# Kernel tuning notes

Hardware: AMD Instinct MI355X
Metric: run time of the kernel (lower is better)

Reference implementation:

```python
import jax, jax.numpy as jnp
import numpy as np

B, S, D, H = 2, 2048, 1024, 16
HD = D // H                      # 64
NUM_ROPE_DIMS = 2
NF = HD // (2 * NUM_ROPE_DIMS)   # 16 freqs per rope dim -> total HD//2
FFN_H = 4 * D


def householder_matrix(vs):
    """Product of Householder reflections: Q = prod_i (I - 2 v_i v_i^T / ||v_i||^2)."""
    dim = vs.shape[-1]
    def step(Q, v):
        v = v[:, None]
        Q = Q - (2.0 / (jnp.sum(v * v) + 1e-8)) * (v @ (v.T @ Q))
        return Q, None
    Q, _ = jax.lax.scan(step, jnp.eye(dim, dtype=vs.dtype), vs)
    return Q


def rmsnorm(x):
    # torch.nn.RMSNorm(eps=None) uses dtype eps, no affine
    return x * jax.lax.rsqrt(jnp.mean(x * x, axis=-1, keepdims=True) + jnp.finfo(x.dtype).eps)


def setup_inputs() -> dict:
    key = jax.random.key(0)
    ks = jax.random.split(key, 8)
    x = jax.random.normal(ks[0], (B, S, D), jnp.float32)
    mask = jnp.tril(jnp.ones((S, S), dtype=bool))          # causal block mask
    qkv_w = jax.random.normal(ks[1], (3 * D, D), jnp.float32) * 0.02
    out_w = jax.random.normal(ks[2], (D, D), jnp.float32) * 0.02
    gate_w = jax.random.normal(ks[3], (D, D), jnp.float32) * 0.02
    gate_b = jnp.zeros((D,), jnp.float32)
    w12 = jax.random.normal(ks[4], (2 * FFN_H, D), jnp.float32) * 0.02
    w3 = jax.random.normal(ks[5], (D, FFN_H), jnp.float32) * 0.02
    hh_vs = jax.random.normal(ks[6], (HD // 2, HD), jnp.float32) * 0.02
    inv_freq = 1.0 / (10000.0 ** (jnp.arange(NF, dtype=jnp.float32) / NF))
    pos = jnp.arange(S, dtype=jnp.float32)
    rope_pos = jnp.stack([pos, pos], axis=-1)              # [S, num_rope_dims]
    return dict(x=x, mask=mask, qkv_w=qkv_w, out_w=out_w, gate_w=gate_w,
                gate_b=gate_b, w12=w12, w3=w3, hh_vs=hh_vs,
                inv_freq=inv_freq, rope_pos=rope_pos)


def reference(x, mask, qkv_w, out_w, gate_w, gate_b, w12, w3, hh_vs, inv_freq, rope_pos):
    Bs, Ss, Ds = x.shape
    resid = x
    xn = rmsnorm(x)
    qkv = xn @ qkv_w.T                                      # [B,S,3D]
    q, k, v = jnp.split(qkv, 3, axis=-1)
    q = q.reshape(Bs, Ss, H, HD).transpose(0, 2, 1, 3)      # [B,H,S,HD]
    k = k.reshape(Bs, Ss, H, HD).transpose(0, 2, 1, 3)
    v = v.reshape(Bs, Ss, H, HD).transpose(0, 2, 1, 3)

    # RnRoPE: rotate into canonical basis, apply RoPE, rotate back
    Q = householder_matrix(hh_vs)                           # [HD,HD]
    q = q @ Q.T
    k = k @ Q.T
    # geo_state.scale = 1.0
    full = jnp.einsum('sd,f->sdf', rope_pos, inv_freq).reshape(Ss, -1)  # [S, HD//2]
    half = HD // 2
    full = full[:, :half]
    emb = jnp.concatenate([full, full], axis=-1)            # [S, HD]
    cos, sin = jnp.cos(emb), jnp.sin(emb)

    def rot(t):
        t1, t2 = jnp.split(t, 2, axis=-1)
        return t * cos + jnp.concatenate([-t2, t1], axis=-1) * sin

    q = rot(q) @ Q
    k = rot(k) @ Q

    # block-masked attention (flex_attention default scale = 1/sqrt(HD))
    scores = jnp.einsum('bhsd,bhtd->bhst', q, k) / jnp.sqrt(jnp.asarray(HD, x.dtype))
    scores = jnp.where(mask, scores, -jnp.inf)
    attn = jax.nn.softmax(scores, axis=-1)
    o = jnp.einsum('bhst,bhtd->bhsd', attn, v)
    o = o.transpose(0, 2, 1, 3).reshape(Bs, Ss, Ds)
    o = o @ out_w.T
    gate = jax.nn.sigmoid(o @ gate_w.T + gate_b)
    x = resid + o * gate

    # SwiGLU FFN
    resid2 = x
    xn2 = rmsnorm(x)
    x12 = xn2 @ w12.T
    x1, x2 = jnp.split(x12, 2, axis=-1)
    ffn = (jax.nn.silu(x1) * x2) @ w3.T
    return resid2 + ffn
```

## Files before the change

### kernel.cpp

```cpp
#include <hip/hip_runtime.h>
#include <hip/hip_bf16.h>
#include <math.h>

constexpr int Bc = 2, Sc = 2048, Dc = 1024, Hc = 16, HDc = 64;
constexpr int D3 = 3 * Dc;

typedef __bf16 bf16x8 __attribute__((ext_vector_type(8)));
typedef float f32x4 __attribute__((ext_vector_type(4)));

__device__ __forceinline__ void gll16(const void* g, void* l) {
  __builtin_amdgcn_global_load_lds((const __attribute__((address_space(1))) unsigned int*)g,
                                   (__attribute__((address_space(3))) unsigned int*)l,
                                   16, 0, 0);
}

__device__ __forceinline__ unsigned short f2bf(float v) {
  __hip_bfloat16 h = __float2bfloat16(v);
  return *(unsigned short*)&h;
}
__device__ __forceinline__ float b2f(unsigned short u) {
  unsigned v = ((unsigned)u) << 16;
  return __uint_as_float(v);
}

#define SBAR() asm volatile("s_barrier" ::: "memory")

__global__ __launch_bounds__(64) void hh_kernel(const float* __restrict__ vs,
                                                float* __restrict__ Qout) {
  __shared__ float Qm[64][65];
  __shared__ float vsh[64];
  int t = threadIdx.x;
  for (int i = 0; i < 64; ++i) Qm[i][t] = (i == t) ? 1.0f : 0.0f;
  for (int it = 0; it < 32; ++it) {
    __syncthreads();
    vsh[t] = vs[it * 64 + t];
    __syncthreads();
    float nv = 0.0f;
    for (int i = 0; i < 64; ++i) nv += vsh[i] * vsh[i];
    float c = 2.0f / (nv + 1e-8f);
    float wj = 0.0f;
    for (int i = 0; i < 64; ++i) wj += vsh[i] * Qm[i][t];
    for (int i = 0; i < 64; ++i) Qm[i][t] -= c * vsh[i] * wj;
  }
  __syncthreads();
  for (int i = 0; i < 64; ++i) Qout[i * 64 + t] = Qm[i][t];
}

__global__ __launch_bounds__(256) void prep_kernel(const float* __restrict__ qkv_w,
                                                   const float* __restrict__ out_w,
                                                   const float* __restrict__ w3,
                                                   const float* __restrict__ gate_w,
                                                   const float* __restrict__ rope_pos,
                                                   const float* __restrict__ inv_freq,
                                                   const float* __restrict__ Qm,
                                                   float2* __restrict__ rtab,
                                                   unsigned short* __restrict__ wqkvb,
                                                   unsigned short* __restrict__ woutb,
                                                   unsigned short* __restrict__ w3b,
                                                   unsigned short* __restrict__ wgateb) {
  const int blk = blockIdx.x;
  const int t = threadIdx.x;
  if (blk < 256) {
    int id = blk * 256 + t;
    int s = id >> 5, d = id & 31;
    float pos = rope_pos[s * 2 + (d >> 4)];
    float emb = pos * inv_freq[d & 15];
    rtab[id] = make_float2(cosf(emb), sinf(emb));
  } else if (blk < 512) {
    __shared__ float qs[64 * 64];
    const int gid = blk - 256;
    const int g = gid >> 3;
    const int c = gid & 7;
    const int base = g * 64;
#pragma unroll
    for (int i = 0; i < 16; ++i) qs[t + i * 256] = Qm[t + i * 256];
    __syncthreads();
    const int tj = t & 127;
    const int rh = (t >> 7) * 32;
    const int col = c * 128 + tj;
    float acc[32] = {};
    const float* wp = qkv_w + (size_t)base * 1024 + col;
    for (int e = 0; e < 64; ++e) {
      float wv = wp[(size_t)e * 1024];
#pragma unroll
      for (int r = 0; r < 32; ++r) acc[r] += qs[(rh + r) * 64 + e] * wv;
    }
    const float sc = (base < 1024) ? 0.18033688f : 1.0f;
#pragma unroll
    for (int r = 0; r < 32; ++r)
      wqkvb[(size_t)(base + rh + r) * 1024 + col] = f2bf(acc[r] * sc);
  } else {
    const float* in;
    unsigned short* out;
    int i;
    if (blk < 1536) {
      in = qkv_w + (size_t)2048 * 1024;
      out = wqkvb + (size_t)2048 * 1024;
      i = (blk - 512) * 256 + t;
    } else if (blk < 2560) {
      in = out_w; out = woutb;
      i = (blk - 1536) * 256 + t;
    } else if (blk < 6656) {
      in = w3; out = w3b;
      i = (blk - 2560) * 256 + t;
    } else {
      in = gate_w; out = wgateb;
      i = (blk - 6656) * 256 + t;
    }
    float4 v = ((const float4*)in)[i];
    ushort4 o;
    o.x = f2bf(v.x); o.y = f2bf(v.y); o.z = f2bf(v.z); o.w = f2bf(v.w);
    ((ushort4*)out)[i] = o;
  }
}

__device__ __forceinline__ void rms_body(const float* __restrict__ in,
                                         unsigned short* __restrict__ out, int row, int t) {
  const float4* x4 = (const float4*)(in + (size_t)row * Dc);
  float4 v = x4[t];
  float s = v.x * v.x + v.y * v.y + v.z * v.z + v.w * v.w;
#pragma unroll
  for (int off = 1; off < 64; off <<= 1) s += __shfl_xor(s, off);
  __shared__ float wsum[4];
  if ((t & 63) == 0) wsum[t >> 6] = s;
  __syncthreads();
  float tot = wsum[0] + wsum[1] + wsum[2] + wsum[3];
  float r = rsqrtf(tot * (1.0f / Dc) + 1.1920928955078125e-07f);
  ushort4 o;
  o.x = f2bf(v.x * r); o.y = f2bf(v.y * r); o.z = f2bf(v.z * r); o.w = f2bf(v.w * r);
  ((ushort4*)(out + (size_t)row * Dc))[t] = o;
}

__global__ __launch_bounds__(256) void rmsnorm_bf16_kernel(const float* __restrict__ in,
                                                           unsigned short* __restrict__ out) {
  rms_body(in, out, blockIdx.x, threadIdx.x);
}

__global__ __launch_bounds__(256) void ropevt_kernel(const unsigned short* __restrict__ qkv,
                                                     const float2* __restrict__ tab,
                                                     unsigned short* __restrict__ qb,
                                                     unsigned short* __restrict__ kb,
                                                     unsigned short* __restrict__ vtb) {
  __shared__ unsigned short tile[64 * 72];
  const int blk = blockIdx.x;
  const int t = threadIdx.x;
  if (blk < 2048) {
    int gid = blk * 64 + (t >> 2);
    int sub = t & 3;
    int h = gid & 15;
    int which = (gid >> 4) & 1;
    int tok = gid >> 5;
    int s = tok & (Sc - 1), b = tok >> 11;
    const unsigned short* src = qkv + (size_t)tok * D3 + which * Dc + h * 64 + sub * 8;
    uint4 lov = *(const uint4*)src;
    uint4 hiv = *(const uint4*)(src + 32);
    const unsigned short* lp = (const unsigned short*)&lov;
    const unsigned short* hp = (const unsigned short*)&hiv;
    unsigned short olo[8], ohi[8];
    const float2* tp = tab + s * 32 + sub * 8;
#pragma unroll
    for (int i = 0; i < 8; ++i) {
      float2 cs = tp[i];
      float lo = b2f(lp[i]), hi = b2f(hp[i]);
      olo[i] = f2bf(lo * cs.x - hi * cs.y);
      ohi[i] = f2bf(hi * cs.x + lo * cs.y);
    }
    unsigned short* dst = (which ? kb : qb) + ((size_t)((b * Hc + h) * Sc + s)) * 64 + sub * 8;
    *(uint4*)dst = *(uint4*)olo;
    *(uint4*)(dst + 32) = *(uint4*)ohi;
  } else {
    int v = blk - 2048;
    int st = v & 31;
    int bh = v >> 5;
    int b = bh >> 4, h = bh & 15;
    int srow = t >> 2, c16 = (t & 3) * 16;
    const unsigned short* src =
        qkv + (size_t)(b * Sc + st * 64 + srow) * D3 + 2 * Dc + h * 64 + c16;
    uint4 a0 = *(const uint4*)src;
    uint4 a1 = *(const uint4*)(src + 8);
    *(uint4*)(tile + srow * 72 + c16) = a0;
    *(uint4*)(tile + srow * 72 + c16 + 8) = a1;
    __syncthreads();
    int d = t >> 2, sch = (t & 3) * 16;
    unsigned short tmp[16];
#pragma unroll
    for (int i = 0; i < 16; ++i) tmp[i] = tile[(sch + i) * 72 + d];
    unsigned short* dst = vtb + ((size_t)(bh * 64 + d)) * Sc + st * 64 + sch;
    *(uint4*)dst = *(uint4*)tmp;
    *(uint4*)(dst + 8) = *(uint4*)(tmp + 8);
  }
}

template <int MODE>
__global__ __launch_bounds__(512, 1) void mgemm8p(const unsigned short* __restrict__ A,
                                                  const unsigned short* __restrict__ B,
                                                  unsigned short* __restrict__ C,
                                                  int M, int N, int K) {
  __shared__ unsigned short lds[65536];
  const int t = threadIdx.x;
  const int lane = t & 63;
  const int wave = t >> 6;
  const int wr = wave >> 2, wc = wave & 3;
  const int l15 = lane & 15, l4 = lane >> 4;
  const int gx = gridDim.x;
  const int nwg = gx * gridDim.y;
  const int id = blockIdx.y * gx + blockIdx.x;
  const int swz = (id & 7) * (nwg >> 3) + (id >> 3);
  const int m0 = (swz / gx) * 256;
  const int n0 = (swz % gx) * 256;
  const int NT = K >> 6;
  const int sko = (((t & 3) ^ ((t >> 3) & 3)) * 8);
  const unsigned short* ag0 = A + (size_t)(m0 + (t >> 2)) * K + sko;
  const unsigned short* ag1 = ag0 + (size_t)128 * K;
  const unsigned short* bg0 = B + (size_t)(n0 + (t >> 2)) * K + sko;
  const unsigned short* bg1 = bg0 + (size_t)128 * K;
  const int t8 = t * 8;
  const int ks = (l4 ^ ((l15 >> 1) & 3)) * 8;
  gll16(ag0, lds + t8);
  gll16(ag1, lds + 4096 + t8);
  gll16(bg0, lds + 32768 + t8);
  gll16(bg1, lds + 32768 + 4096 + t8);
  gll16(ag0 + 32, lds + 8192 + t8);
  gll16(ag1 + 32, lds + 8192 + 4096 + t8);
  gll16(bg0 + 32, lds + 32768 + 8192 + t8);
  gll16(bg1 + 32, lds + 32768 + 8192 + 4096 + t8);
  asm volatile("s_waitcnt vmcnt(4)" ::: "memory");
  SBAR();
  f32x4 acc[8][4] = {};
  for (int kt = 0; kt < NT; ++kt) {
    const int cur = (kt & 1) << 14;
    const int nxt = cur ^ 16384;
    const int kof = ((kt + 1 < NT) ? (kt + 1) : kt) << 6;
    const unsigned short* Ap = lds + cur;
    const unsigned short* Bp = lds + 32768 + cur;
    bf16x8 a[8], b0, b1;
#pragma unroll
    for (int i = 0; i < 8; ++i)
      a[i] = *(const bf16x8*)(Ap + (wr * 128 + i * 16 + l15) * 32 + ks);
    b0 = *(const bf16x8*)(Bp + (wc * 64 + l15) * 32 + ks);
    b1 = *(const bf16x8*)(Bp + (wc * 64 + 16 + l15) * 32 + ks);
    gll16(ag0 + kof, lds + nxt + t8);
    gll16(ag1 + kof, lds + nxt + 4096 + t8);
    SBAR();
    __builtin_amdgcn_s_setprio(1);
#pragma unroll
    for (int i = 0; i < 8; ++i) {
      acc[i][0] = __builtin_amdgcn_mfma_f32_16x16x32_bf16(a[i], b0, acc[i][0], 0, 0, 0);
      acc[i][1] = __builtin_amdgcn_mfma_f32_16x16x32_bf16(a[i], b1, acc[i][1], 0, 0, 0);
    }
    __builtin_amdgcn_s_setprio(0);
    SBAR();
    b0 = *(const bf16x8*)(Bp + (wc * 64 + 32 + l15) * 32 + ks);
    b1 = *(const bf16x8*)(Bp + (wc * 64 + 48 + l15) * 32 + ks);
    gll16(bg0 + kof, lds + 32768 + nxt + t8);
    gll16(bg1 + kof, lds + 32768 + nxt + 4096 + t8);
    asm volatile("s_waitcnt vmcnt(4)" ::: "memory");
    SBAR();
    __builtin_amdgcn_s_setprio(1);
#pragma unroll
    for (int i = 0; i < 8; ++i) {
      acc[i][2] = __builtin_amdgcn_mfma_f32_16x16x32_bf16(a[i], b0, acc[i][2], 0, 0, 0);
      acc[i][3] = __builtin_amdgcn_mfma_f32_16x16x32_bf16(a[i], b1, acc[i][3], 0, 0, 0);
    }
    __builtin_amdgcn_s_setprio(0);
    SBAR();
#pragma unroll
    for (int i = 0; i < 8; ++i)
      a[i] = *(const bf16x8*)(Ap + 8192 + (wr * 128 + i * 16 + l15) * 32 + ks);
    b0 = *(const bf16x8*)(Bp + 8192 + (wc * 64 + l15) * 32 + ks);
    b1 = *(const bf16x8*)(Bp + 8192 + (wc * 64 + 16 + l15) * 32 + ks);
    gll16(ag0 + kof + 32, lds + nxt + 8192 + t8);
    gll16(ag1 + kof + 32, lds + nxt + 8192 + 4096 + t8);
    SBAR();
    __builtin_amdgcn_s_setprio(1);
#pragma unroll
    for (int i = 0; i < 8; ++i) {
      acc[i][0] = __builtin_amdgcn_mfma_f32_16x16x32_bf16(a[i], b0, acc[i][0], 0, 0, 0);
      acc[i][1] = __builtin_amdgcn_mfma_f32_16x16x32_bf16(a[i], b1, acc[i][1], 0, 0, 0);
    }
    __builtin_amdgcn_s_setprio(0);
    SBAR();
    b0 = *(const bf16x8*)(Bp + 8192 + (wc * 64 + 32 + l15) * 32 + ks);
    b1 = *(const bf16x8*)(Bp + 8192 + (wc * 64 + 48 + l15) * 32 + ks);
    gll16(bg0 + kof + 32, lds + 32768 + nxt + 8192 + t8);
    gll16(bg1 + kof + 32, lds + 32768 + nxt + 8192 + 4096 + t8);
    asm volatile("s_waitcnt vmcnt(4)" ::: "memory");
    SBAR();
    __builtin_amdgcn_s_setprio(1);
#pragma unroll
    for (int i = 0; i < 8; ++i) {
      acc[i][2] = __builtin_amdgcn_mfma_f32_16x16x32_bf16(a[i], b0, acc[i][2], 0, 0, 0);
      acc[i][3] = __builtin_amdgcn_mfma_f32_16x16x32_bf16(a[i], b1, acc[i][3], 0, 0, 0);
    }
    __builtin_amdgcn_s_setprio(0);
    SBAR();
  }
  asm volatile("s_waitcnt vmcnt(0)" ::: "memory");
  const int r0 = m0 + wr * 128 + l4 * 4;
  if (MODE == 0) {
    const int c0 = n0 + wc * 64 + l15;
#pragma unroll
    for (int i = 0; i < 8; ++i)
#pragma unroll
      for (int j = 0; j < 4; ++j)
#pragma unroll
        for (int r = 0; r < 4; ++r)
          C[(size_t)(r0 + i * 16 + r) * N + c0 + j * 16] = f2bf(acc[i][j][r]);
  } else {
    const int nc = N >> 1;
    const int c0 = (n0 >> 1) + wc * 32 + l15;
#pragma unroll
    for (int i = 0; i < 8; ++i)
#pragma unroll
      for (int p = 0; p < 2; ++p)
#pragma unroll
        for (int r = 0; r < 4; ++r) {
          float v = acc[i][2 * p][r];
          float sv = v / (1.0f + __expf(-v));
          C[(size_t)(r0 + i * 16 + r) * nc + c0 + p * 16] = f2bf(sv * acc[i][2 * p + 1][r]);
        }
  }
}

template <int MODE>
__global__ __launch_bounds__(256, 2) void mgemm64(const unsigned short* __restrict__ A,
                                                  const unsigned short* __restrict__ W,
                                                  const float* __restrict__ R,
                                                  const float* __restrict__ R2,
                                                  const float* __restrict__ bias,
                                                  void* __restrict__ Cout,
                                                  void* __restrict__ Cout2,
                                                  int M, int N, int K) {
  __shared__ unsigned short As[3][2][2048];
  __shared__ unsigned short Bs[3][2][4096];
  const int t = threadIdx.x;
  const int lane = t & 63;
  const int wave = t >> 6;
  const int wr = wave >> 1, wc = wave & 1;
  const int gx = gridDim.x;
  const int nwg = gx * gridDim.y;
  const int id = blockIdx.y * gx + blockIdx.x;
  const int swz = (id & 7) * (nwg >> 3) + (id >> 3);
  const int m0 = (swz / gx) * 64, n0 = (swz % gx) * 128;
  f32x4 acc[2][4] = {};
  const int srow = t >> 2;
  const int sch = (((t & 3) ^ ((t >> 3) & 3)) * 8);
  const unsigned short* Ag = A + (size_t)(m0 + srow) * K + sch;
  const unsigned short* Wg = W + (size_t)(n0 + srow) * K + sch;
  const size_t rstep = (size_t)64 * K;
  const int frow = lane & 15;
  const int l4 = lane >> 4;
  const int fk = (l4 ^ ((frow >> 1) & 3)) * 8;
  const int t8 = t * 8;
#pragma unroll
  for (int p = 0; p < 2; ++p) {
    const int ko = p * 64;
    gll16(Ag + ko, As[p][0] + t8);
    gll16(Ag + ko + 32, As[p][1] + t8);
    gll16(Wg + ko, Bs[p][0] + t8);
    gll16(Wg + ko + rstep, Bs[p][0] + 2048 + t8);
    gll16(Wg + ko + 32, Bs[p][1] + t8);
    gll16(Wg + ko + rstep + 32, Bs[p][1] + 2048 + t8);
  }
  const int NS = K >> 6;
  for (int s = 0; s < NS; ++s) {
    const int cur = s % 3;
    const int nxt = (s + 2) % 3;
    const int kn = (s + 2 < NS) ? (s + 2) * 64 : s * 64;
    gll16(Ag + kn, As[nxt][0] + t8);
    gll16(Ag + kn + 32, As[nxt][1] + t8);
    gll16(Wg + kn, Bs[nxt][0] + t8);
    gll16(Wg + kn + rstep, Bs[nxt][0] + 2048 + t8);
    gll16(Wg + kn + 32, Bs[nxt][1] + t8);
    gll16(Wg + kn + rstep + 32, Bs[nxt][1] + 2048 + t8);
    asm volatile("s_waitcnt vmcnt(12)" ::: "memory");
    SBAR();
#pragma unroll
    for (int kh = 0; kh < 2; ++kh) {
      bf16x8 af[2], bq[4];
#pragma unroll
      for (int i = 0; i < 2; ++i)
        af[i] = *(const bf16x8*)(As[cur][kh] + (wr * 32 + i * 16 + frow) * 32 + fk);
#pragma unroll
      for (int j = 0; j < 4; ++j)
        bq[j] = *(const bf16x8*)(Bs[cur][kh] + (wc * 64 + j * 16 + frow) * 32 + fk);
      __builtin_amdgcn_s_setprio(1);
#pragma unroll
      for (int i = 0; i < 2; ++i)
#pragma unroll
        for (int j = 0; j < 4; ++j)
          acc[i][j] = __builtin_amdgcn_mfma_f32_16x16x32_bf16(af[i], bq[j], acc[i][j], 0, 0, 0);
      __builtin_amdgcn_s_setprio(0);
    }
    SBAR();
  }
  asm volatile("s_waitcnt vmcnt(0)" ::: "memory");
  const int crow = wr * 32 + (lane >> 4) * 4;
  const int ccol = wc * 64 + (lane & 15);
#pragma unroll
  for (int i = 0; i < 2; ++i) {
#pragma unroll
    for (int j = 0; j < 4; ++j) {
#pragma unroll
      for (int r = 0; r < 4; ++r) {
        int row = m0 + crow + i * 16 + r;
        int col = n0 + ccol + j * 16;
        float v = acc[i][j][r];
        size_t off = (size_t)row * N + col;
        if (MODE == 2) {
          ((float*)Cout)[off] = v + R[off];
        } else if (MODE == 4) {
          ((float*)Cout)[off] = v;
          ((unsigned short*)Cout2)[off] = f2bf(v);
        } else {
          float g = v + bias[col];
          float sg = 1.0f / (1.0f + __expf(-g));
          ((float*)Cout)[off] = R[off] + R2[off] * sg;
        }
      }
    }
  }
}

__global__ __launch_bounds__(256, 3) void mattn(const unsigned short* __restrict__ qb,
                                                const unsigned short* __restrict__ kb,
                                                const unsigned short* __restrict__ vtb,
                                                unsigned short* __restrict__ opart,
                                                float* __restrict__ lpart,
                                                const float* __restrict__ w12,
                                                unsigned short* __restrict__ w12b) {
  __shared__ unsigned short Ks[2][4096];
  __shared__ unsigned short Vts[2][4096];
  __shared__ unsigned short Ps[4 * 16 * 72];
  const int t = threadIdx.x;
  if (blockIdx.x >= 40) {
    const int r = (blockIdx.x - 40) * 32 + blockIdx.y;
    const int g = r >> 5, u = r & 31;
    const int src = ((u < 16) ? 0 : 4096) + g * 16 + (u & 15);
    float4 v = ((const float4*)(w12 + (size_t)src * 1024))[t];
    ushort4 o;
    o.x = f2bf(v.x); o.y = f2bf(v.y); o.z = f2bf(v.z); o.w = f2bf(v.w);
    ((ushort4*)(w12b + (size_t)r * 1024))[t] = o;
    return;
  }
  const int bidx = 39 - blockIdx.x;
  int qt, s;
  if (bidx < 4)       { qt = bidx;                  s = 0; }
  else if (bidx < 12) { qt = 4 + ((bidx - 4) >> 1); s = (bidx - 4) & 1; }
  else if (bidx < 24) { int u = bidx - 12; int q3 = u / 3; qt = 8 + q3; s = u - 3 * q3; }
  else                { qt = 12 + ((bidx - 24) >> 2); s = (bidx - 24) & 3; }
  const int nt = 2 * qt + 2;
  const int kt0 = s * 8;
  const int kt1 = (kt0 + 8 < nt) ? kt0 + 8 : nt;
  const int bh = blockIdx.y;
  const int lane = t & 63, w = t >> 6;
  const int l15 = lane & 15, l4 = lane >> 4;
  const unsigned short* qbase = qb + ((size_t)bh * Sc + qt * 128) * 64;
  const unsigned short* kbase = kb + (size_t)bh * Sc * 64;
  const unsigned short* vbase = vtb + (size_t)bh * 64 * Sc;
  bf16x8 qf[2][2];
#pragma unroll
  for (int ch = 0; ch < 2; ++ch)
#pragma unroll
    for (int kc = 0; kc < 2; ++kc)
      qf[ch][kc] = *(const bf16x8*)(qbase + (size_t)(ch * 64 + w * 16 + l15) * 64 +
                                    (kc * 4 + l4) * 8);
  const int sr = t >> 3;
  const int scg = (t & 7) ^ (sr & 7);
  gll16(kbase + (size_t)(kt0 * 64 + sr) * 64 + scg * 8, Ks[0] + t * 8);
  gll16(kbase + (size_t)(kt0 * 64 + sr + 32) * 64 + scg * 8, Ks[0] + 2048 + t * 8);
  gll16(vbase + (size_t)sr * Sc + kt0 * 64 + scg * 8, Vts[0] + t * 8);
  gll16(vbase + (size_t)(sr + 32) * Sc + kt0 * 64 + scg * 8, Vts[0] + 2048 + t * 8);
  f32x4 oacc[2][4] = {};
  float lrow[2][4] = {};
  unsigned short* pw = Ps + w * 16 * 72;
  for (int kt = kt0; kt < kt1; ++kt) {
    const int cur = (kt - kt0) & 1;
    const int ktn = (kt + 1 < kt1) ? kt + 1 : kt;
    gll16(kbase + (size_t)(ktn * 64 + sr) * 64 + scg * 8, Ks[cur ^ 1] + t * 8);
    gll16(kbase + (size_t)(ktn * 64 + sr + 32) * 64 + scg * 8, Ks[cur ^ 1] + 2048 + t * 8);
    gll16(vbase + (size_t)sr * Sc + ktn * 64 + scg * 8, Vts[cur ^ 1] + t * 8);
    gll16(vbase + (size_t)(sr + 32) * Sc + ktn * 64 + scg * 8, Vts[cur ^ 1] + 2048 + t * 8);
    asm volatile("s_waitcnt vmcnt(4)" ::: "memory");
    SBAR();
    const bool actA = (kt <= 2 * qt);
    f32x4 sc[2][4] = {};
#pragma unroll
    for (int kc = 0; kc < 2; ++kc) {
      bf16x8 kf[4];
#pragma unroll
      for (int j = 0; j < 4; ++j)
        kf[j] = *(const bf16x8*)(Ks[cur] + (j * 16 + l15) * 64 + (((kc * 4 + l4) ^ (l15 & 7)) * 8));
      __builtin_amdgcn_s_setprio(1);
      if (actA) {
#pragma unroll
        for (int j = 0; j < 4; ++j)
          sc[0][j] = __builtin_amdgcn_mfma_f32_16x16x32_bf16(qf[0][kc], kf[j], sc[0][j], 0, 0, 0);
      }
#pragma unroll
      for (int j = 0; j < 4; ++j)
        sc[1][j] = __builtin_amdgcn_mfma_f32_16x16x32_bf16(qf[1][kc], kf[j], sc[1][j], 0, 0, 0);
      __builtin_amdgcn_s_setprio(0);
    }
    const int rl = w * 16 + l4 * 4;
    if (kt == 2 * qt) {
#pragma unroll
      for (int j = 0; j < 4; ++j)
#pragma unroll
        for (int r = 0; r < 4; ++r)
          if (j * 16 + l15 > rl + r) sc[0][j][r] = -INFINITY;
    }
    if (kt == 2 * qt + 1) {
#pragma unroll
      for (int j = 0; j < 4; ++j)
#pragma unroll
        for (int r = 0; r < 4; ++r)
          if (j * 16 + l15 > rl + r) sc[1][j][r] = -INFINITY;
    }
    bf16x8 vf[2][4];
#pragma unroll
    for (int kc = 0; kc < 2; ++kc)
#pragma unroll
      for (int j = 0; j < 4; ++j)
        vf[kc][j] = *(const bf16x8*)(Vts[cur] + (j * 16 + l15) * 64 + (((kc * 4 + l4) ^ (l15 & 7)) * 8));
#pragma unroll
    for (int ch = 0; ch < 2; ++ch) {
      if (ch == 0 && !actA) continue;
#pragma unroll
      for (int j = 0; j < 4; ++j)
#pragma unroll
        for (int r = 0; r < 4; ++r) {
          float p = exp2f(sc[ch][j][r]);
          lrow[ch][r] += p;
          pw[(l4 * 4 + r) * 72 + j * 16 + l15] = f2bf(p);
        }
      __asm__ __volatile__("s_waitcnt lgkmcnt(0)" ::: "memory");
      __builtin_amdgcn_s_setprio(1);
#pragma unroll
      for (int kc = 0; kc < 2; ++kc) {
        bf16x8 pf = *(const bf16x8*)(pw + l15 * 72 + kc * 32 + l4 * 8);
#pragma unroll
        for (int j = 0; j < 4; ++j)
          oacc[ch][j] = __builtin_amdgcn_mfma_f32_16x16x32_bf16(pf, vf[kc][j], oacc[ch][j], 0, 0, 0);
      }
      __builtin_amdgcn_s_setprio(0);
    }
    SBAR();
  }
  asm volatile("s_waitcnt vmcnt(0)" ::: "memory");
  unsigned short* opr = opart + ((size_t)(bh * 40 + bidx) * 128) * 64;
  float* lpr = lpart + (bh * 40 + bidx) * 128;
#pragma unroll
  for (int ch = 0; ch < 2; ++ch) {
#pragma unroll
    for (int r = 0; r < 4; ++r) {
      float sum = lrow[ch][r];
      sum += __shfl_xor(sum, 1);
      sum += __shfl_xor(sum, 2);
      sum += __shfl_xor(sum, 4);
      sum += __shfl_xor(sum, 8);
      const int row = ch * 64 + w * 16 + l4 * 4 + r;
      if (l15 == 0) lpr[row] = sum;
#pragma unroll
      for (int j = 0; j < 4; ++j)
        opr[(size_t)row * 64 + j * 16 + l15] = f2bf(oacc[ch][j][r]);
    }
  }
}

__global__ __launch_bounds__(256) void acomb(const unsigned short* __restrict__ Op,
                                             const float* __restrict__ lp,
                                             unsigned short* __restrict__ out) {
  const int qt = blockIdx.x, bh = blockIdx.y;
  const int b = bh >> 4, h = bh & 15;
  const int ns = (qt >> 2) + 1;
  const int base = (qt < 4) ? qt
                 : (qt < 8) ? 4 + 2 * (qt - 4)
                 : (qt < 12) ? 12 + 3 * (qt - 8)
                 : 24 + 4 * (qt - 12);
  const int t = threadIdx.x;
  const int row = t >> 1, d0 = (t & 1) * 32;
  float l = 0.0f;
  float acc[32] = {};
  for (int s = 0; s < ns; ++s) {
    const int pidx = bh * 40 + base + s;
    l += lp[pidx * 128 + row];
    const unsigned short* src = Op + ((size_t)pidx * 128 + row) * 64 + d0;
#pragma unroll
    for (int i = 0; i < 4; ++i) {
      uint4 v = *(const uint4*)(src + i * 8);
      const unsigned short* e = (const unsigned short*)&v;
#pragma unroll
      for (int j = 0; j < 8; ++j) acc[i * 8 + j] += b2f(e[j]);
    }
  }
  const float inv = 1.0f / l;
  unsigned short* dst = out + ((size_t)(b * Sc + qt * 128 + row)) * Dc + h * 64 + d0;
#pragma unroll
  for (int i = 0; i < 8; ++i) {
    ushort4 o;
    o.x = f2bf(acc[i * 4 + 0] * inv); o.y = f2bf(acc[i * 4 + 1] * inv);
    o.z = f2bf(acc[i * 4 + 2] * inv); o.w = f2bf(acc[i * 4 + 3] * inv);
    ((ushort4*)dst)[i] = o;
  }
}

extern "C" void kernel_launch(void* const* d_in, const int* in_sizes, int n_in,
                              void* d_out, int out_size, void* d_ws, size_t ws_size,
                              hipStream_t stream) {
  const float* x        = (const float*)d_in[0];
  const float* qkv_w    = (const float*)d_in[2];
  const float* out_w    = (const float*)d_in[3];
  const float* gate_w   = (const float*)d_in[4];
  const float* gate_b   = (const float*)d_in[5];
  const float* w12      = (const float*)d_in[6];
  const float* w3       = (const float*)d_in[7];
  const float* hh_vs    = (const float*)d_in[8];
  const float* inv_freq = (const float*)d_in[9];
  const float* rope_pos = (const float*)d_in[10];
  char* ws = (char*)d_ws;
  unsigned short* woutb  = (unsigned short*)(ws + 0);
  float2*         rtab   = (float2*)(ws + 2097152);
  unsigned short* wqkvb  = (unsigned short*)(ws + 4194304);
  unsigned short* attnb  = (unsigned short*)(ws + 4194304);
  float*          lpart  = (float*)(ws + 12582912);
  float*          xmid   = (float*)(ws + 0);
  unsigned short* slotB  = (unsigned short*)(ws + 16777216);
  unsigned short* opart  = (unsigned short*)(ws + 16777216);
  float*          oproj  = (float*)(ws + 25165824);
  unsigned short* w3b    = (unsigned short*)(ws + 41943040);
  unsigned short* wgateb = (unsigned short*)(ws + 50331648);
  unsigned short* qkvb   = (unsigned short*)(ws + 58720256);
  unsigned short* w12b   = (unsigned short*)(ws + 58720256);
  unsigned short* hbufb  = (unsigned short*)(ws + 75497472);
  unsigned short* qb     = (unsigned short*)(ws + 83886080);
  unsigned short* oprojb = (unsigned short*)(ws + 83886080);
  unsigned short* kb     = (unsigned short*)(ws + 92274688);
  unsigned short* vtb    = (unsigned short*)(ws + 100663296);
  float*          Qb     = (float*)(ws + 109051904);
  float* outp = (float*)d_out;

  hh_kernel<<<1, 64, 0, stream>>>(hh_vs, Qb);
  prep_kernel<<<7680, 256, 0, stream>>>(qkv_w, out_w, w3, gate_w, rope_pos, inv_freq, Qb,
                                        rtab, wqkvb, woutb, w3b, wgateb);
  rmsnorm_bf16_kernel<<<4096, 256, 0, stream>>>(x, slotB);
  mgemm8p<0><<<dim3(12, 16), 512, 0, stream>>>(slotB, wqkvb, qkvb, 4096, 3072, 1024);
  ropevt_kernel<<<3072, 256, 0, stream>>>(qkvb, rtab, qb, kb, vtb);
  mattn<<<dim3(296, 32), 256, 0, stream>>>(qb, kb, vtb, opart, lpart, w12, w12b);
  acomb<<<dim3(16, 32), 256, 0, stream>>>(opart, lpart, attnb);
  mgemm64<4><<<dim3(8, 64), 256, 0, stream>>>(attnb, woutb, nullptr, nullptr, nullptr,
                                              oproj, oprojb, 4096, 1024, 1024);
  mgemm64<5><<<dim3(8, 64), 256, 0, stream>>>(oprojb, wgateb, x, oproj, gate_b,
                                              xmid, nullptr, 4096, 1024, 1024);
  rmsnorm_bf16_kernel<<<4096, 256, 0, stream>>>(xmid, slotB);
  mgemm8p<1><<<dim3(32, 16), 512, 0, stream>>>(slotB, w12b, hbufb, 4096, 8192, 1024);
  mgemm64<2><<<dim3(8, 64), 256, 0, stream>>>(hbufb, w3b, xmid, nullptr, nullptr,
                                              outp, nullptr, 4096, 1024, 4096);
}
```

Baseline: 485.1 us.

## Fuse first rmsnorm into prep and move weight casts into attention kernel

The first RMSNorm is folded into the prep kernel as extra blocks, which removes one kernel launch. The fp32-to-bf16 casts of out_w, w3 and gate_w move out of prep and into extra blocks of the attention kernel. That way they run alongside attention instead of ahead of the QKV GEMM on the critical path. The grid grows from 296 to 488 in x, and the cast blocks compete with attention blocks for CUs and memory bandwidth. Those weights are only read after attention finishes, so the ordering stays correct.

```diff
diff --git a/kernel.cpp b/kernel.cpp
--- a/kernel.cpp
+++ b/kernel.cpp
@@ -46,18 +46,36 @@
   for (int i = 0; i < 64; ++i) Qout[i * 64 + t] = Qm[i][t];
 }
 
+__device__ __forceinline__ void rms_body(const float* __restrict__ in,
+                                         unsigned short* __restrict__ out, int row, int t) {
+  const float4* x4 = (const float4*)(in + (size_t)row * Dc);
+  float4 v = x4[t];
+  float s = v.x * v.x + v.y * v.y + v.z * v.z + v.w * v.w;
+#pragma unroll
+  for (int off = 1; off < 64; off <<= 1) s += __shfl_xor(s, off);
+  __shared__ float wsum[4];
+  if ((t & 63) == 0) wsum[t >> 6] = s;
+  __syncthreads();
+  float tot = wsum[0] + wsum[1] + wsum[2] + wsum[3];
+  float r = rsqrtf(tot * (1.0f / Dc) + 1.1920928955078125e-07f);
+  ushort4 o;
+  o.x = f2bf(v.x * r); o.y = f2bf(v.y * r); o.z = f2bf(v.z * r); o.w = f2bf(v.w * r);
+  ((ushort4*)(out + (size_t)row * Dc))[t] = o;
+}
+
+__global__ __launch_bounds__(256) void rmsnorm_bf16_kernel(const float* __restrict__ in,
+                                                           unsigned short* __restrict__ out) {
+  rms_body(in, out, blockIdx.x, threadIdx.x);
+}
+
 __global__ __launch_bounds__(256) void prep_kernel(const float* __restrict__ qkv_w,
-                                                   const float* __restrict__ out_w,
-                                                   const float* __restrict__ w3,
-                                                   const float* __restrict__ gate_w,
                                                    const float* __restrict__ rope_pos,
                                                    const float* __restrict__ inv_freq,
                                                    const float* __restrict__ Qm,
+                                                   const float* __restrict__ x,
                                                    float2* __restrict__ rtab,
                                                    unsigned short* __restrict__ wqkvb,
-                                                   unsigned short* __restrict__ woutb,
-                                                   unsigned short* __restrict__ w3b,
-                                                   unsigned short* __restrict__ wgateb) {
+                                                   unsigned short* __restrict__ xn) {
   const int blk = blockIdx.x;
   const int t = threadIdx.x;
   if (blk < 256) {
@@ -89,51 +107,15 @@
 #pragma unroll
     for (int r = 0; r < 32; ++r)
       wqkvb[(size_t)(base + rh + r) * 1024 + col] = f2bf(acc[r] * sc);
-  } else {
-    const float* in;
-    unsigned short* out;
-    int i;
-    if (blk < 1536) {
-      in = qkv_w + (size_t)2048 * 1024;
-      out = wqkvb + (size_t)2048 * 1024;
-      i = (blk - 512) * 256 + t;
-    } else if (blk < 2560) {
-      in = out_w; out = woutb;
-      i = (blk - 1536) * 256 + t;
-    } else if (blk < 6656) {
-      in = w3; out = w3b;
-      i = (blk - 2560) * 256 + t;
-    } else {
-      in = gate_w; out = wgateb;
-      i = (blk - 6656) * 256 + t;
-    }
-    float4 v = ((const float4*)in)[i];
+  } else if (blk < 1536) {
+    int i = (blk - 512) * 256 + t;
+    float4 v = ((const float4*)(qkv_w + (size_t)2048 * 1024))[i];
     ushort4 o;
     o.x = f2bf(v.x); o.y = f2bf(v.y); o.z = f2bf(v.z); o.w = f2bf(v.w);
-    ((ushort4*)out)[i] = o;
-  }
-}
-
-__device__ __forceinline__ void rms_body(const float* __restrict__ in,
-                                         unsigned short* __restrict__ out, int row, int t) {
-  const float4* x4 = (const float4*)(in + (size_t)row * Dc);
-  float4 v = x4[t];
-  float s = v.x * v.x + v.y * v.y + v.z * v.z + v.w * v.w;
-#pragma unroll
-  for (int off = 1; off < 64; off <<= 1) s += __shfl_xor(s, off);
-  __shared__ float wsum[4];
-  if ((t & 63) == 0) wsum[t >> 6] = s;
-  __syncthreads();
-  float tot = wsum[0] + wsum[1] + wsum[2] + wsum[3];
-  float r = rsqrtf(tot * (1.0f / Dc) + 1.1920928955078125e-07f);
-  ushort4 o;
-  o.x = f2bf(v.x * r); o.y = f2bf(v.y * r); o.z = f2bf(v.z * r); o.w = f2bf(v.w * r);
-  ((ushort4*)(out + (size_t)row * Dc))[t] = o;
-}
-
-__global__ __launch_bounds__(256) void rmsnorm_bf16_kernel(const float* __restrict__ in,
-                                                           unsigned short* __restrict__ out) {
-  rms_body(in, out, blockIdx.x, threadIdx.x);
+    ((ushort4*)(wqkvb + (size_t)2048 * 1024))[i] = o;
+  } else {
+    rms_body(x, xn, blk - 1536, t);
+  }
 }
 
 __global__ __launch_bounds__(256) void ropevt_kernel(const unsigned short* __restrict__ qkv,
@@ -428,11 +410,35 @@
                                                 unsigned short* __restrict__ opart,
                                                 float* __restrict__ lpart,
                                                 const float* __restrict__ w12,
-                                                unsigned short* __restrict__ w12b) {
+                                                unsigned short* __restrict__ w12b,
+                                                const float* __restrict__ out_w,
+                                                unsigned short* __restrict__ woutb,
+                                                const float* __restrict__ w3,
+                                                unsigned short* __restrict__ w3b,
+                                                const float* __restrict__ gate_w,
+                                                unsigned short* __restrict__ wgateb) {
   __shared__ unsigned short Ks[2][4096];
   __shared__ unsigned short Vts[2][4096];
   __shared__ unsigned short Ps[4 * 16 * 72];
   const int t = threadIdx.x;
+  if (blockIdx.x >= 296) {
+    const int cb = (blockIdx.x - 296) * 32 + blockIdx.y;
+    const float* in;
+    unsigned short* out;
+    int i;
+    if (cb < 1024) {
+      in = out_w; out = woutb; i = cb * 256 + t;
+    } else if (cb < 5120) {
+      in = w3; out = w3b; i = (cb - 1024) * 256 + t;
+    } else {
+      in = gate_w; out = wgateb; i = (cb - 5120) * 256 + t;
+    }
+    float4 v = ((const float4*)in)[i];
+    ushort4 o;
+    o.x = f2bf(v.x); o.y = f2bf(v.y); o.z = f2bf(v.z); o.w = f2bf(v.w);
+    ((ushort4*)out)[i] = o;
+    return;
+  }
   if (blockIdx.x >= 40) {
     const int r = (blockIdx.x - 40) * 32 + blockIdx.y;
     const int g = r >> 5, u = r & 31;
@@ -641,12 +647,12 @@
   float* outp = (float*)d_out;
 
   hh_kernel<<<1, 64, 0, stream>>>(hh_vs, Qb);
-  prep_kernel<<<7680, 256, 0, stream>>>(qkv_w, out_w, w3, gate_w, rope_pos, inv_freq, Qb,
-                                        rtab, wqkvb, woutb, w3b, wgateb);
-  rmsnorm_bf16_kernel<<<4096, 256, 0, stream>>>(x, slotB);
+  prep_kernel<<<5632, 256, 0, stream>>>(qkv_w, rope_pos, inv_freq, Qb, x,
+                                        rtab, wqkvb, slotB);
   mgemm8p<0><<<dim3(12, 16), 512, 0, stream>>>(slotB, wqkvb, qkvb, 4096, 3072, 1024);
   ropevt_kernel<<<3072, 256, 0, stream>>>(qkvb, rtab, qb, kb, vtb);
-  mattn<<<dim3(296, 32), 256, 0, stream>>>(qb, kb, vtb, opart, lpart, w12, w12b);
+  mattn<<<dim3(488, 32), 256, 0, stream>>>(qb, kb, vtb, opart, lpart, w12, w12b,
+                                           out_w, woutb, w3, w3b, gate_w, wgateb);
   acomb<<<dim3(16, 32), 256, 0, stream>>>(opart, lpart, attnb);
   mgemm64<4><<<dim3(8, 64), 256, 0, stream>>>(attnb, woutb, nullptr, nullptr, nullptr,
                                               oproj, oprojb, 4096, 1024, 1024);
```

Measured after the change: 492.3 us. Within noise of the previous version (+1.5%).
